# Performance work log

Measured on AMD Instinct MI355X. Metric: run time of the kernel, lower is better.

Reference implementation:

```python
import jax, jax.numpy as jnp
import numpy as np

H = 12   # num_attention_heads
T = 8    # sample_num (frames)
D = 768  # hidden_size


def ln(x, g, b, eps=1e-12):
    m = x.mean(-1, keepdims=True)
    v = x.var(-1, keepdims=True)
    return (x - m) / jnp.sqrt(v + eps) * g + b


def attn(q, k, v):
    # q: [..., Q, Dh], k/v: [..., K, Dh]
    d = q.shape[-1]
    s = jnp.einsum('...qd,...kd->...qk', q, k) / jnp.sqrt(jnp.asarray(d, q.dtype))
    a = jax.nn.softmax(s, axis=-1)
    return jnp.einsum('...qk,...kd->...qd', a, v)


def mha_divided(x, Wq, bq, Wk, bk, Wv, bv, Wo, bo, mode):
    B, S, Dm = x.shape
    Dh = Dm // H
    P = (S - 1) // T

    def proj(W, b):
        return (x @ W + b).reshape(B, S, H, Dh).transpose(0, 2, 1, 3)  # [B,H,S,Dh]

    q, k, v = proj(Wq, bq), proj(Wk, bk), proj(Wv, bv)

    # cls token attends over the full sequence
    cls_ctx = attn(q[:, :, 0:1], k, v)                       # [B,H,1,Dh]
    cls_out = cls_ctx.transpose(0, 2, 1, 3).reshape(B, 1, Dm) @ Wo + bo

    qp = q[:, :, 1:].reshape(B, H, T, P, Dh)
    kp = k[:, :, 1:].reshape(B, H, T, P, Dh)
    vp = v[:, :, 1:].reshape(B, H, T, P, Dh)
    kc, vc = k[:, :, 0], v[:, :, 0]                          # [B,H,Dh]

    if mode == 'time':
        # each patch attends over [cls] + same patch across T frames
        qt = qp.transpose(0, 1, 3, 2, 4)                     # [B,H,P,T,Dh]
        kt = jnp.concatenate([jnp.broadcast_to(kc[:, :, None, None], (B, H, P, 1, Dh)),
                              kp.transpose(0, 1, 3, 2, 4)], axis=3)  # [B,H,P,T+1,Dh]
        vt = jnp.concatenate([jnp.broadcast_to(vc[:, :, None, None], (B, H, P, 1, Dh)),
                              vp.transpose(0, 1, 3, 2, 4)], axis=3)
        ctx = attn(qt, kt, vt)                               # [B,H,P,T,Dh]
        out = ctx.transpose(0, 3, 2, 1, 4).reshape(B, T * P, Dm)  # [B,T,P,H,Dh]
    else:  # 'space': each frame attends over [cls] + P patches in that frame
        kt = jnp.concatenate([jnp.broadcast_to(kc[:, :, None, None], (B, H, T, 1, Dh)), kp], axis=3)
        vt = jnp.concatenate([jnp.broadcast_to(vc[:, :, None, None], (B, H, T, 1, Dh)), vp], axis=3)
        ctx = attn(qp, kt, vt)                               # [B,H,T,P,Dh]
        out = ctx.transpose(0, 2, 3, 1, 4).reshape(B, T * P, Dm)
    out = out @ Wo + bo
    return jnp.concatenate([cls_out, out], axis=1)


def _forward(hidden_states,
             t_Wq, t_bq, t_Wk, t_bk, t_Wv, t_bv, t_Wo, t_bo,
             s_Wq, s_bq, s_Wk, s_bk, s_Wv, s_bv, s_Wo, s_bo,
             W1, b1, W2, b2,
             ln1_g, ln1_b, ln2_g, ln2_b, ln3_g, ln3_b):
    x = hidden_states
    # divided time attention
    x = x + mha_divided(ln(x, ln1_g, ln1_b), t_Wq, t_bq, t_Wk, t_bk, t_Wv, t_bv, t_Wo, t_bo, 'time')
    # divided space attention
    x = x + mha_divided(ln(x, ln2_g, ln2_b), s_Wq, s_bq, s_Wk, s_bk, s_Wv, s_bv, s_Wo, s_bo, 'space')
    # feed-forward with exact (erf) GELU
    h = ln(x, ln3_g, ln3_b)
    x = x + jax.nn.gelu(h @ W1 + b1, approximate=False) @ W2 + b2
    return x


def setup_inputs() -> dict:
    key = jax.random.key(0)
    ks = jax.random.split(key, 16)

    def w(k, shape, s=0.02):
        return jax.random.normal(k, shape, jnp.float32) * s

    B, S = 8, 1 + T * 196
    inp = {"hidden_states": jax.random.normal(ks[0], (B, S, D), jnp.float32)}
    names = ["t_Wq", "t_Wk", "t_Wv", "t_Wo", "s_Wq", "s_Wk", "s_Wv", "s_Wo"]
    for i, n in enumerate(names):
        inp[n] = w(ks[1 + i], (D, D))
        inp[n.replace("W", "b")] = jnp.zeros((D,), jnp.float32)
    inp["W1"] = w(ks[9], (D, 4 * D)); inp["b1"] = jnp.zeros((4 * D,), jnp.float32)
    inp["W2"] = w(ks[10], (4 * D, D)); inp["b2"] = jnp.zeros((D,), jnp.float32)
    for i in (1, 2, 3):
        inp[f"ln{i}_g"] = jnp.ones((D,), jnp.float32)
        inp[f"ln{i}_b"] = jnp.zeros((D,), jnp.float32)
    return inp


def reference(hidden_states,
              t_Wq, t_bq, t_Wk, t_bk, t_Wv, t_bv, t_Wo, t_bo,
              s_Wq, s_bq, s_Wk, s_bk, s_Wv, s_bv, s_Wo, s_bo,
              W1, b1, W2, b2,
              ln1_g, ln1_b, ln2_g, ln2_b, ln3_g, ln3_b):
    return _forward(hidden_states,
                    t_Wq, t_bq, t_Wk, t_bk, t_Wv, t_bv, t_Wo, t_bo,
                    s_Wq, s_bq, s_Wk, s_bk, s_Wv, s_bv, s_Wo, s_bo,
                    W1, b1, W2, b2,
                    ln1_g, ln1_b, ln2_g, ln2_b, ln3_g, ln3_b)
```

## Files before the change

### kernel.cpp

```cpp
#include <hip/hip_runtime.h>

#define BQ   8
#define SQ   1569
#define BS   12552
#define DM   768
#define NH   12
#define DH   64
#define TT   8
#define PP   196
#define D4   3072
#define QKVN 2304
#define CCH  24
#define CKEY 66
#define MB_PAD 104

typedef _Float16 f16;
typedef _Float16 f16x8 __attribute__((ext_vector_type(8)));
typedef float    f32x4 __attribute__((ext_vector_type(4)));
typedef unsigned long long u64;

#define AS1 __attribute__((address_space(1)))
#define AS3 __attribute__((address_space(3)))

#define Y_OFF    0ULL
#define QKV_OFF  19279872ULL
#define CTX_OFF  77119488ULL
#define H_OFF    19279872ULL
#define W_OFF    96399360ULL

__global__ __launch_bounds__(256) void ln_kernel(const float* __restrict__ x,
                                                 const float* __restrict__ g,
                                                 const float* __restrict__ bta,
                                                 f16* __restrict__ y) {
    int row = blockIdx.x * 4 + (threadIdx.x >> 6);
    int lane = threadIdx.x & 63;
    if (row >= BS) return;
    const float* xr = x + (u64)row * DM;
    float v[12];
    float s = 0.f, s2 = 0.f;
#pragma unroll
    for (int i = 0; i < 12; i++) { v[i] = xr[lane + i * 64]; s += v[i]; s2 += v[i] * v[i]; }
#pragma unroll
    for (int m = 1; m < 64; m <<= 1) { s += __shfl_xor(s, m, 64); s2 += __shfl_xor(s2, m, 64); }
    float mean = s * (1.f / 768.f);
    float var  = s2 * (1.f / 768.f) - mean * mean;
    float rstd = rsqrtf(var + 1e-12f);
    f16* yr = y + (u64)row * DM;
#pragma unroll
    for (int i = 0; i < 12; i++) {
        int c = lane + i * 64;
        yr[c] = (f16)((v[i] - mean) * rstd * g[c] + bta[c]);
    }
}

__global__ __launch_bounds__(256) void transpose_kernel(const float* __restrict__ src,
                                                        f16* __restrict__ dst,
                                                        int R, int C) {
    __shared__ float tile[32][33];
    int bx = blockIdx.x * 32;
    int by = blockIdx.y * 32;
    int tx = threadIdx.x & 31, ty = threadIdx.x >> 5;
#pragma unroll
    for (int i = 0; i < 4; i++) {
        int r = by + ty + i * 8, c = bx + tx;
        if (r < R && c < C) tile[ty + i * 8][tx] = src[(u64)r * C + c];
    }
    __syncthreads();
#pragma unroll
    for (int i = 0; i < 4; i++) {
        int c = bx + ty + i * 8, r = by + tx;
        if (c < C && r < R) dst[(u64)c * R + r] = (f16)tile[tx][ty + i * 8];
    }
}

__global__ __launch_bounds__(256) void bias3_kernel(const float* __restrict__ a,
                                                    const float* __restrict__ b,
                                                    const float* __restrict__ c,
                                                    float* __restrict__ dst) {
    int i = blockIdx.x * 256 + threadIdx.x;
    if (i < 768) { dst[i] = a[i]; dst[i + 768] = b[i]; dst[i + 1536] = c[i]; }
}

template <int NOUT, bool GELU, bool RESID, bool OUTF16>
__global__ __launch_bounds__(256, 3) void gemm_kernel(const f16* __restrict__ A,
                                                      const f16* __restrict__ Bt,
                                                      const float* __restrict__ bias,
                                                      const float* __restrict__ resid,
                                                      float* __restrict__ Cf,
                                                      f16* __restrict__ Ch,
                                                      int K) {
    __shared__ __align__(16) f16 As[3][128 * 32];
    __shared__ __align__(16) f16 Bs[3][128 * 32];
    int id = blockIdx.x;
    int mb = id % MB_PAD, nb = id / MB_PAD;
    if (mb >= 99) return;
    int tid  = threadIdx.x;
    int lane = tid & 63, wave = tid >> 6;
    int wm = wave >> 1, wn = wave & 1;
    int m0 = mb * 128, n0 = nb * 128;
    int l15 = lane & 15, quad = lane >> 4;

    int r0   = wave * 16 + (lane >> 2);
    int coff = (((lane & 3) ^ ((lane >> 3) & 3))) * 8;
    int ra0 = m0 + r0;       if (ra0 > BS - 1) ra0 = BS - 1;
    int ra1 = m0 + r0 + 64;  if (ra1 > BS - 1) ra1 = BS - 1;
    const f16* ag0 = A + (u64)ra0 * K + coff;
    const f16* ag1 = A + (u64)ra1 * K + coff;
    const f16* bg0 = Bt + (u64)(n0 + r0) * K + coff;
    const f16* bg1 = Bt + (u64)(n0 + r0 + 64) * K + coff;
    int lofs = wave * 1024;

    int gsw = (quad ^ ((l15 >> 1) & 3)) * 8;

#define STAGE(BUF, KT) { \
    u64 _ko = (u64)(KT) * 32; \
    __builtin_amdgcn_global_load_lds((const AS1 void*)(ag0 + _ko), (AS3 void*)((AS3 char*)&As[BUF][0] + lofs), 16, 0, 0); \
    __builtin_amdgcn_global_load_lds((const AS1 void*)(ag1 + _ko), (AS3 void*)((AS3 char*)&As[BUF][0] + lofs + 4096), 16, 0, 0); \
    __builtin_amdgcn_global_load_lds((const AS1 void*)(bg0 + _ko), (AS3 void*)((AS3 char*)&Bs[BUF][0] + lofs), 16, 0, 0); \
    __builtin_amdgcn_global_load_lds((const AS1 void*)(bg1 + _ko), (AS3 void*)((AS3 char*)&Bs[BUF][0] + lofs + 4096), 16, 0, 0); \
}

    f32x4 acc[4][4];
#pragma unroll
    for (int i = 0; i < 4; i++)
#pragma unroll
        for (int j = 0; j < 4; j++)
#pragma unroll
            for (int r = 0; r < 4; r++) acc[i][j][r] = 0.f;

    STAGE(0, 0);
    STAGE(1, 1);

    int nit = K >> 5;
    int cbuf = 0, sbuf = 2;
    for (int it = 0; it < nit; it++) {
        if (it + 1 < nit) { asm volatile("s_waitcnt vmcnt(4)"); }
        else              { asm volatile("s_waitcnt vmcnt(0)"); }
        __builtin_amdgcn_s_barrier();
        __builtin_amdgcn_sched_barrier(0);
        if (it + 2 < nit) STAGE(sbuf, it + 2);

        f16x8 af[4], bf[4];
#pragma unroll
        for (int i = 0; i < 4; i++)
            af[i] = *(const f16x8*)(&As[cbuf][(wm * 64 + i * 16 + l15) * 32 + gsw]);
#pragma unroll
        for (int j = 0; j < 4; j++)
            bf[j] = *(const f16x8*)(&Bs[cbuf][(wn * 64 + j * 16 + l15) * 32 + gsw]);
#pragma unroll
        for (int i = 0; i < 4; i++)
#pragma unroll
            for (int j = 0; j < 4; j++)
                acc[i][j] = __builtin_amdgcn_mfma_f32_16x16x32_f16(af[i], bf[j], acc[i][j], 0, 0, 0);

        cbuf = (cbuf == 2) ? 0 : cbuf + 1;
        sbuf = (sbuf == 2) ? 0 : sbuf + 1;
    }
#undef STAGE

#pragma unroll
    for (int i = 0; i < 4; i++) {
#pragma unroll
        for (int j = 0; j < 4; j++) {
            int col = n0 + wn * 64 + j * 16 + l15;
            float bv = bias[col];
#pragma unroll
            for (int r = 0; r < 4; r++) {
                int row = m0 + wm * 64 + i * 16 + quad * 4 + r;
                if (row < BS) {
                    float v = acc[i][j][r] + bv;
                    if (GELU) {
                        float u = 0.7978845608028654f * (v + 0.044715f * v * v * v);
                        float e = __builtin_exp2f(-2.885390081777927f * u);
                        v = v / (1.f + e);
                    }
                    if (RESID) v += resid[(u64)row * NOUT + col];
                    if (OUTF16) Ch[(u64)row * NOUT + col] = (f16)v;
                    else        Cf[(u64)row * NOUT + col] = v;
                }
            }
        }
    }
}

__global__ __launch_bounds__(256) void time_attn_kernel(const f16* __restrict__ qkv,
                                                        f16* __restrict__ ctx) {
    int w = blockIdx.x * 4 + (threadIdx.x >> 6);
    int lane = threadIdx.x & 63;
    int b = w / (NH * PP);
    int rem = w % (NH * PP);
    int h = rem / PP, p = rem % PP;
    u64 bb = (u64)b * SQ;
    int hoff = h * 64 + lane;

    float qv[TT], kv[9], vv[9];
#pragma unroll
    for (int t = 0; t < TT; t++) qv[t] = (float)qkv[(bb + 1 + t * PP + p) * QKVN + hoff];
    kv[0] = (float)qkv[bb * QKVN + 768 + hoff];
    vv[0] = (float)qkv[bb * QKVN + 1536 + hoff];
#pragma unroll
    for (int j = 1; j <= TT; j++) {
        u64 ro = (bb + 1 + (u64)(j - 1) * PP + p) * QKVN;
        kv[j] = (float)qkv[ro + 768 + hoff];
        vv[j] = (float)qkv[ro + 1536 + hoff];
    }
#pragma unroll
    for (int t = 0; t < TT; t++) {
        float s[9];
#pragma unroll
        for (int j = 0; j < 9; j++) {
            float ps = qv[t] * kv[j];
#pragma unroll
            for (int m = 1; m < 64; m <<= 1) ps += __shfl_xor(ps, m, 64);
            s[j] = ps * 0.125f;
        }
        float mx = s[0];
#pragma unroll
        for (int j = 1; j < 9; j++) mx = fmaxf(mx, s[j]);
        float sum = 0.f;
#pragma unroll
        for (int j = 0; j < 9; j++) { s[j] = expf(s[j] - mx); sum += s[j]; }
        float o = 0.f;
#pragma unroll
        for (int j = 0; j < 9; j++) o += s[j] * vv[j];
        o /= sum;
        ctx[(bb + 1 + (u64)t * PP + p) * DM + h * 64 + lane] = (f16)o;
    }
}

__global__ __launch_bounds__(256) void cls_part_kernel(const f16* __restrict__ qkv,
                                                       float* __restrict__ part) {
    int g = blockIdx.x;
    int c = g % CCH, bh = g / CCH;
    int b = bh / NH, h = bh % NH;
    u64 bb = (u64)b * SQ;
    int tid = threadIdx.x, lane = tid & 63, wave = tid >> 6;
    __shared__ float sc[CKEY];
    __shared__ float accbuf[4][64];
    __shared__ float lbuf[4];
    __shared__ float mxs;
    float qd = (float)qkv[bb * QKVN + h * 64 + lane];
    int j0 = c * CKEY;
    int cnt = SQ - j0; if (cnt > CKEY) cnt = CKEY;
    for (int jj = wave; jj < cnt; jj += 4) {
        float p = qd * (float)qkv[(bb + j0 + jj) * QKVN + 768 + h * 64 + lane];
#pragma unroll
        for (int m = 1; m < 64; m <<= 1) p += __shfl_xor(p, m, 64);
        if (lane == 0) sc[jj] = p * 0.125f;
    }
    __syncthreads();
    if (wave == 0) {
        float m = -1e30f;
        for (int j = lane; j < cnt; j += 64) m = fmaxf(m, sc[j]);
#pragma unroll
        for (int s = 1; s < 64; s <<= 1) m = fmaxf(m, __shfl_xor(m, s, 64));
        if (lane == 0) mxs = m;
    }
    __syncthreads();
    float mx = mxs;
    float acc = 0.f, l = 0.f;
    for (int jj = wave; jj < cnt; jj += 4) {
        float w = expf(sc[jj] - mx);
        l += w;
        acc += w * (float)qkv[(bb + j0 + jj) * QKVN + 1536 + h * 64 + lane];
    }
    accbuf[wave][lane] = acc;
    if (lane == 0) lbuf[wave] = l;
    __syncthreads();
    if (tid < 64) {
        float a = accbuf[0][tid] + accbuf[1][tid] + accbuf[2][tid] + accbuf[3][tid];
        float* pb = part + ((u64)bh * CCH + c) * 66;
        if (tid == 0) { pb[0] = mxs; pb[1] = lbuf[0] + lbuf[1] + lbuf[2] + lbuf[3]; }
        pb[2 + tid] = a;
    }
}

__global__ __launch_bounds__(256) void cls_comb_kernel(const float* __restrict__ part,
                                                       f16* __restrict__ ctx) {
    int w = blockIdx.x * 4 + (threadIdx.x >> 6);
    int lane = threadIdx.x & 63;
    if (w >= BQ * NH) return;
    int b = w / NH, h = w % NH;
    const float* pb = part + (u64)w * CCH * 66;
    float m = (lane < CCH) ? pb[lane * 66] : -1e30f;
#pragma unroll
    for (int s = 1; s < 64; s <<= 1) m = fmaxf(m, __shfl_xor(m, s, 64));
    float l = (lane < CCH) ? pb[lane * 66 + 1] * expf(pb[lane * 66] - m) : 0.f;
#pragma unroll
    for (int s = 1; s < 64; s <<= 1) l += __shfl_xor(l, s, 64);
    float o = 0.f;
    for (int j = 0; j < CCH; j++) {
        float mj = pb[j * 66];
        o += pb[j * 66 + 2 + lane] * expf(mj - m);
    }
    ctx[((u64)b * SQ) * DM + h * 64 + lane] = (f16)(o / l);
}

__global__ __launch_bounds__(256) void space_attn_kernel(const f16* __restrict__ qkv,
                                                         f16* __restrict__ ctx) {
    int g = blockIdx.x;
    int b = g / (NH * TT);
    int rem = g % (NH * TT);
    int h = rem / TT, t = rem % TT;
    __shared__ __align__(16) f16 Vt[64 * 232];
    __shared__ __align__(16) f16 Ps[4 * 16 * 232];
    u64 bb = (u64)b * SQ;
    int tid = threadIdx.x, lane = tid & 63, wave = tid >> 6;
    int l15 = lane & 15, quad = lane >> 4;

    for (int i = tid; i < 4 * 16 * 232 * 2 / 16; i += 256)
        ((uint4*)Ps)[i] = make_uint4(0u, 0u, 0u, 0u);

    for (int idx = tid; idx < 232 * 8; idx += 256) {
        int c8 = idx / 232;
        int j  = idx - c8 * 232;
        int c  = c8 * 8;
        uint4 vraw = make_uint4(0u, 0u, 0u, 0u);
        if (j < 197) {
            int tok = (j == 0) ? 0 : (1 + t * PP + (j - 1));
            vraw = *(const uint4*)(qkv + (bb + tok) * QKVN + 1536 + h * 64 + c);
        }
        f16x8 vv = *(f16x8*)&vraw;
#pragma unroll
        for (int e = 0; e < 8; e++) Vt[(c + e) * 232 + j] = vv[e];
    }
    __syncthreads();

    f16* myP = Ps + wave * 16 * 232;
    for (int qt = wave; qt < 13; qt += 4) {
        int mloc = qt * 16 + l15;
        int mc = mloc > 195 ? 195 : mloc;
        const f16* qr = qkv + (bb + 1 + (u64)t * PP + mc) * QKVN + h * 64;
        f16x8 qa0 = *(const f16x8*)(qr + quad * 8);
        f16x8 qa1 = *(const f16x8*)(qr + 32 + quad * 8);

        f32x4 s[13];
#pragma unroll
        for (int nt = 0; nt < 13; nt++) { s[nt][0] = 0.f; s[nt][1] = 0.f; s[nt][2] = 0.f; s[nt][3] = 0.f; }
#pragma unroll
        for (int nt = 0; nt < 13; nt++) {
            int n = nt * 16 + l15;
            int ncl = n > 196 ? 196 : n;
            int tok = (ncl == 0) ? 0 : (1 + t * PP + (ncl - 1));
            const f16* kr = qkv + (bb + tok) * QKVN + 768 + h * 64;
            f16x8 kb0 = *(const f16x8*)(kr + quad * 8);
            f16x8 kb1 = *(const f16x8*)(kr + 32 + quad * 8);
            s[nt] = __builtin_amdgcn_mfma_f32_16x16x32_f16(qa0, kb0, s[nt], 0, 0, 0);
            s[nt] = __builtin_amdgcn_mfma_f32_16x16x32_f16(qa1, kb1, s[nt], 0, 0, 0);
        }
        if (l15 >= 5) { s[12][0] = -1e30f; s[12][1] = -1e30f; s[12][2] = -1e30f; s[12][3] = -1e30f; }

        float mx[4] = {-1e30f, -1e30f, -1e30f, -1e30f};
#pragma unroll
        for (int nt = 0; nt < 13; nt++)
#pragma unroll
            for (int r = 0; r < 4; r++) mx[r] = fmaxf(mx[r], s[nt][r]);
#pragma unroll
        for (int m = 1; m < 16; m <<= 1)
#pragma unroll
            for (int r = 0; r < 4; r++) mx[r] = fmaxf(mx[r], __shfl_xor(mx[r], m, 64));

        float sum[4] = {0.f, 0.f, 0.f, 0.f};
#pragma unroll
        for (int nt = 0; nt < 13; nt++)
#pragma unroll
            for (int r = 0; r < 4; r++) {
                float p = exp2f((s[nt][r] - mx[r]) * 0.18033688011112042f);
                s[nt][r] = p;
                sum[r] += p;
            }
#pragma unroll
        for (int m = 1; m < 16; m <<= 1)
#pragma unroll
            for (int r = 0; r < 4; r++) sum[r] += __shfl_xor(sum[r], m, 64);

#pragma unroll
        for (int nt = 0; nt < 13; nt++)
#pragma unroll
            for (int r = 0; r < 4; r++)
                myP[(quad * 4 + r) * 232 + nt * 16 + l15] = (f16)s[nt][r];

        f32x4 o[4];
#pragma unroll
        for (int n2 = 0; n2 < 4; n2++) { o[n2][0] = 0.f; o[n2][1] = 0.f; o[n2][2] = 0.f; o[n2][3] = 0.f; }
#pragma unroll
        for (int kc = 0; kc < 7; kc++) {
            f16x8 pa = *(const f16x8*)(&myP[l15 * 232 + kc * 32 + quad * 8]);
#pragma unroll
            for (int n2 = 0; n2 < 4; n2++) {
                f16x8 vb = *(const f16x8*)(&Vt[(n2 * 16 + l15) * 232 + kc * 32 + quad * 8]);
                o[n2] = __builtin_amdgcn_mfma_f32_16x16x32_f16(pa, vb, o[n2], 0, 0, 0);
            }
        }

        float inv[4];
#pragma unroll
        for (int r = 0; r < 4; r++) inv[r] = 1.f / sum[r];
#pragma unroll
        for (int n2 = 0; n2 < 4; n2++)
#pragma unroll
            for (int r = 0; r < 4; r++) {
                int m = qt * 16 + quad * 4 + r;
                if (m < PP)
                    ctx[(bb + 1 + (u64)t * PP + m) * DM + h * 64 + n2 * 16 + l15] = (f16)(o[n2][r] * inv[r]);
            }
    }
}

extern "C" void kernel_launch(void* const* d_in, const int* in_sizes, int n_in,
                              void* d_out, int out_size, void* d_ws, size_t ws_size,
                              hipStream_t stream) {
    const float* x_in  = (const float*)d_in[0];
    const float* t_Wq  = (const float*)d_in[1];
    const float* t_bq  = (const float*)d_in[2];
    const float* t_Wk  = (const float*)d_in[3];
    const float* t_bk  = (const float*)d_in[4];
    const float* t_Wv  = (const float*)d_in[5];
    const float* t_bv  = (const float*)d_in[6];
    const float* t_Wo  = (const float*)d_in[7];
    const float* t_bo  = (const float*)d_in[8];
    const float* s_Wq  = (const float*)d_in[9];
    const float* s_bq  = (const float*)d_in[10];
    const float* s_Wk  = (const float*)d_in[11];
    const float* s_bk  = (const float*)d_in[12];
    const float* s_Wv  = (const float*)d_in[13];
    const float* s_bv  = (const float*)d_in[14];
    const float* s_Wo  = (const float*)d_in[15];
    const float* s_bo  = (const float*)d_in[16];
    const float* W1    = (const float*)d_in[17];
    const float* b1    = (const float*)d_in[18];
    const float* W2    = (const float*)d_in[19];
    const float* b2    = (const float*)d_in[20];
    const float* ln1g  = (const float*)d_in[21];
    const float* ln1b  = (const float*)d_in[22];
    const float* ln2g  = (const float*)d_in[23];
    const float* ln2b  = (const float*)d_in[24];
    const float* ln3g  = (const float*)d_in[25];
    const float* ln3b  = (const float*)d_in[26];

    char* ws = (char*)d_ws;
    f16* y    = (f16*)(ws + Y_OFF);
    f16* qkv  = (f16*)(ws + QKV_OFF);
    f16* ctx  = (f16*)(ws + CTX_OFF);
    f16* hbuf = (f16*)(ws + H_OFF);
    float* clsP = (float*)(ws + Y_OFF);
    char* wreg = ws + W_OFF;
    f16* tQKV  = (f16*)(wreg);
    f16* tWoT  = (f16*)(wreg + 3538944);
    f16* sQKV  = (f16*)(wreg + 4718592);
    f16* sWoT  = (f16*)(wreg + 8257536);
    f16* W1T   = (f16*)(wreg + 9437184);
    f16* W2T   = (f16*)(wreg + 14155776);
    float* tBias = (float*)(wreg + 18874368);
    float* sBias = (float*)(wreg + 18883584);
    float* xcur  = (float*)d_out;

    dim3 tb(256);
    transpose_kernel<<<dim3(24, 24), tb, 0, stream>>>(t_Wq, tQKV, 768, 768);
    transpose_kernel<<<dim3(24, 24), tb, 0, stream>>>(t_Wk, tQKV + 768 * 768, 768, 768);
    transpose_kernel<<<dim3(24, 24), tb, 0, stream>>>(t_Wv, tQKV + 2 * 768 * 768, 768, 768);
    transpose_kernel<<<dim3(24, 24), tb, 0, stream>>>(t_Wo, tWoT, 768, 768);
    transpose_kernel<<<dim3(24, 24), tb, 0, stream>>>(s_Wq, sQKV, 768, 768);
    transpose_kernel<<<dim3(24, 24), tb, 0, stream>>>(s_Wk, sQKV + 768 * 768, 768, 768);
    transpose_kernel<<<dim3(24, 24), tb, 0, stream>>>(s_Wv, sQKV + 2 * 768 * 768, 768, 768);
    transpose_kernel<<<dim3(24, 24), tb, 0, stream>>>(s_Wo, sWoT, 768, 768);
    transpose_kernel<<<dim3(96, 24), tb, 0, stream>>>(W1, W1T, 768, 3072);
    transpose_kernel<<<dim3(24, 96), tb, 0, stream>>>(W2, W2T, 3072, 768);
    bias3_kernel<<<3, tb, 0, stream>>>(t_bq, t_bk, t_bv, tBias);
    bias3_kernel<<<3, tb, 0, stream>>>(s_bq, s_bk, s_bv, sBias);

    ln_kernel<<<3138, tb, 0, stream>>>(x_in, ln1g, ln1b, y);
    gemm_kernel<QKVN, false, false, true><<<MB_PAD * 18, tb, 0, stream>>>(y, tQKV, tBias, nullptr, nullptr, qkv, 768);
    time_attn_kernel<<<4704, tb, 0, stream>>>(qkv, ctx);
    cls_part_kernel<<<BQ * NH * CCH, tb, 0, stream>>>(qkv, clsP);
    cls_comb_kernel<<<24, tb, 0, stream>>>(clsP, ctx);
    gemm_kernel<DM, false, true, false><<<MB_PAD * 6, tb, 0, stream>>>(ctx, tWoT, t_bo, x_in, xcur, nullptr, 768);

    ln_kernel<<<3138, tb, 0, stream>>>(xcur, ln2g, ln2b, y);
    gemm_kernel<QKVN, false, false, true><<<MB_PAD * 18, tb, 0, stream>>>(y, sQKV, sBias, nullptr, nullptr, qkv, 768);
    space_attn_kernel<<<768, tb, 0, stream>>>(qkv, ctx);
    cls_part_kernel<<<BQ * NH * CCH, tb, 0, stream>>>(qkv, clsP);
    cls_comb_kernel<<<24, tb, 0, stream>>>(clsP, ctx);
    gemm_kernel<DM, false, true, false><<<MB_PAD * 6, tb, 0, stream>>>(ctx, sWoT, s_bo, xcur, xcur, nullptr, 768);

    ln_kernel<<<3138, tb, 0, stream>>>(xcur, ln3g, ln3b, y);
    gemm_kernel<D4, true, false, true><<<MB_PAD * 24, tb, 0, stream>>>(y, W1T, b1, nullptr, nullptr, hbuf, 768);
    gemm_kernel<DM, false, true, false><<<MB_PAD * 6, tb, 0, stream>>>(hbuf, W2T, b2, xcur, xcur, nullptr, 3072);
}
```

Baseline: 904.9 us.

## Give each wave private LDS tiles to remove block barriers in GEMM

The GEMM mainloop now has each wave load its own 64-row A and B slices into a per-wave double-buffered LDS region, replacing the block-shared triple buffer. Because no wave reads another wave's data, the per-iteration s_barrier is dropped and only vmcnt/lgkmcnt waits are used. The cost is duplicated global loads, since A and B tiles are each fetched twice across waves, and larger LDS use (64KB) that lowers the occupancy target to 2 blocks per CU.

```diff
diff --git a/kernel.cpp b/kernel.cpp
--- a/kernel.cpp
+++ b/kernel.cpp
@@ -82,15 +82,14 @@
 }
 
 template <int NOUT, bool GELU, bool RESID, bool OUTF16>
-__global__ __launch_bounds__(256, 3) void gemm_kernel(const f16* __restrict__ A,
+__global__ __launch_bounds__(256, 2) void gemm_kernel(const f16* __restrict__ A,
                                                       const f16* __restrict__ Bt,
                                                       const float* __restrict__ bias,
                                                       const float* __restrict__ resid,
                                                       float* __restrict__ Cf,
                                                       f16* __restrict__ Ch,
                                                       int K) {
-    __shared__ __align__(16) f16 As[3][128 * 32];
-    __shared__ __align__(16) f16 Bs[3][128 * 32];
+    __shared__ __align__(16) f16 L[4][2][4096];
     int id = blockIdx.x;
     int mb = id % MB_PAD, nb = id / MB_PAD;
     if (mb >= 99) return;
@@ -100,24 +99,30 @@
     int m0 = mb * 128, n0 = nb * 128;
     int l15 = lane & 15, quad = lane >> 4;
 
-    int r0   = wave * 16 + (lane >> 2);
-    int coff = (((lane & 3) ^ ((lane >> 3) & 3))) * 8;
-    int ra0 = m0 + r0;       if (ra0 > BS - 1) ra0 = BS - 1;
-    int ra1 = m0 + r0 + 64;  if (ra1 > BS - 1) ra1 = BS - 1;
-    const f16* ag0 = A + (u64)ra0 * K + coff;
-    const f16* ag1 = A + (u64)ra1 * K + coff;
-    const f16* bg0 = Bt + (u64)(n0 + r0) * K + coff;
-    const f16* bg1 = Bt + (u64)(n0 + r0 + 64) * K + coff;
-    int lofs = wave * 1024;
-
-    int gsw = (quad ^ ((l15 >> 1) & 3)) * 8;
+    int rq   = lane >> 2;
+    int coff = ((lane & 3) ^ ((lane >> 3) & 3)) * 8;
+    const f16* ag[4];
+    const f16* bg[4];
+#pragma unroll
+    for (int j = 0; j < 4; j++) {
+        int ra = m0 + wm * 64 + j * 16 + rq; if (ra > BS - 1) ra = BS - 1;
+        ag[j] = A + (u64)ra * K + coff;
+        bg[j] = Bt + (u64)(n0 + wn * 64 + j * 16 + rq) * K + coff;
+    }
+    AS3 char* waveL = (AS3 char*)&L[0][0][0] + wave * 16384;
+    int gsw = (quad ^ ((l15 >> 1) & 3)) * 16;
 
 #define STAGE(BUF, KT) { \
     u64 _ko = (u64)(KT) * 32; \
-    __builtin_amdgcn_global_load_lds((const AS1 void*)(ag0 + _ko), (AS3 void*)((AS3 char*)&As[BUF][0] + lofs), 16, 0, 0); \
-    __builtin_amdgcn_global_load_lds((const AS1 void*)(ag1 + _ko), (AS3 void*)((AS3 char*)&As[BUF][0] + lofs + 4096), 16, 0, 0); \
-    __builtin_amdgcn_global_load_lds((const AS1 void*)(bg0 + _ko), (AS3 void*)((AS3 char*)&Bs[BUF][0] + lofs), 16, 0, 0); \
-    __builtin_amdgcn_global_load_lds((const AS1 void*)(bg1 + _ko), (AS3 void*)((AS3 char*)&Bs[BUF][0] + lofs + 4096), 16, 0, 0); \
+    AS3 char* _d = waveL + (BUF) * 8192; \
+    __builtin_amdgcn_global_load_lds((const AS1 void*)(ag[0] + _ko), (AS3 void*)(_d),        16, 0, 0); \
+    __builtin_amdgcn_global_load_lds((const AS1 void*)(ag[1] + _ko), (AS3 void*)(_d + 1024), 16, 0, 0); \
+    __builtin_amdgcn_global_load_lds((const AS1 void*)(ag[2] + _ko), (AS3 void*)(_d + 2048), 16, 0, 0); \
+    __builtin_amdgcn_global_load_lds((const AS1 void*)(ag[3] + _ko), (AS3 void*)(_d + 3072), 16, 0, 0); \
+    __builtin_amdgcn_global_load_lds((const AS1 void*)(bg[0] + _ko), (AS3 void*)(_d + 4096), 16, 0, 0); \
+    __builtin_amdgcn_global_load_lds((const AS1 void*)(bg[1] + _ko), (AS3 void*)(_d + 5120), 16, 0, 0); \
+    __builtin_amdgcn_global_load_lds((const AS1 void*)(bg[2] + _ko), (AS3 void*)(_d + 6144), 16, 0, 0); \
+    __builtin_amdgcn_global_load_lds((const AS1 void*)(bg[3] + _ko), (AS3 void*)(_d + 7168), 16, 0, 0); \
 }
 
     f32x4 acc[4][4];
@@ -132,29 +137,27 @@
     STAGE(1, 1);
 
     int nit = K >> 5;
-    int cbuf = 0, sbuf = 2;
     for (int it = 0; it < nit; it++) {
-        if (it + 1 < nit) { asm volatile("s_waitcnt vmcnt(4)"); }
-        else              { asm volatile("s_waitcnt vmcnt(0)"); }
-        __builtin_amdgcn_s_barrier();
-        __builtin_amdgcn_sched_barrier(0);
-        if (it + 2 < nit) STAGE(sbuf, it + 2);
+        int buf = it & 1;
+        if (it + 1 < nit) { asm volatile("s_waitcnt vmcnt(8)" ::: "memory"); }
+        else              { asm volatile("s_waitcnt vmcnt(0)" ::: "memory"); }
+        const AS3 char* Ap = waveL + buf * 8192;
 
         f16x8 af[4], bf[4];
 #pragma unroll
         for (int i = 0; i < 4; i++)
-            af[i] = *(const f16x8*)(&As[cbuf][(wm * 64 + i * 16 + l15) * 32 + gsw]);
+            af[i] = *(const AS3 f16x8*)(Ap + (i * 16 + l15) * 64 + gsw);
 #pragma unroll
         for (int j = 0; j < 4; j++)
-            bf[j] = *(const f16x8*)(&Bs[cbuf][(wn * 64 + j * 16 + l15) * 32 + gsw]);
+            bf[j] = *(const AS3 f16x8*)(Ap + 4096 + (j * 16 + l15) * 64 + gsw);
+        asm volatile("s_waitcnt lgkmcnt(0)" ::: "memory");
+        if (it + 2 < nit) STAGE(buf, it + 2);
+
 #pragma unroll
         for (int i = 0; i < 4; i++)
 #pragma unroll
             for (int j = 0; j < 4; j++)
                 acc[i][j] = __builtin_amdgcn_mfma_f32_16x16x32_f16(af[i], bf[j], acc[i][j], 0, 0, 0);
-
-        cbuf = (cbuf == 2) ? 0 : cbuf + 1;
-        sbuf = (sbuf == 2) ? 0 : sbuf + 1;
     }
 #undef STAGE
 
```

Result: slower. 1.082 ms (+19.6%).
